# Performance work log

Hardware: AMD Instinct MI355X
Metric: run time of the kernel (lower is better)

Reference implementation:

```python
import jax, jax.numpy as jnp
import numpy as np

EPS = 1e-16  # PyG softmax denominator epsilon


def segment_softmax(alpha, batch, num_segments):
    # alpha: (n,1); softmax within each bag (PyG-style: subtract segment max)
    m = jax.ops.segment_max(alpha, batch, num_segments=num_segments)
    e = jnp.exp(alpha - m[batch])
    s = jax.ops.segment_sum(e, batch, num_segments=num_segments)
    return e / (s[batch] + EPS)


def global_softmax_pooling(x, alpha, batch, num_segments):
    a = segment_softmax(alpha, batch, num_segments)
    return jax.ops.segment_sum(x * a, batch, num_segments=num_segments)  # (B,d)


def setup_inputs() -> dict:
    key = jax.random.key(0)
    k1, k2 = jax.random.split(key)
    n, d, B = 262144, 256, 512
    x = jax.random.normal(k1, (n, d), dtype=jnp.float32)
    batch = jnp.sort(jax.random.randint(k2, (n,), 0, B))
    return {"x": x, "batch": batch, "num_segments": B}


def reference(x, batch, num_segments):
    K = 3  # module default k
    alpha = jnp.zeros((x.shape[0], 1), dtype=x.dtype)
    for _ in range(K):  # small fixed iteration count
        z = global_softmax_pooling(x, alpha, batch, num_segments)  # (B,d)
        energy = jnp.sum(z * z, axis=1, keepdims=True)  # (B,1)
        z_squashed = jnp.sqrt(energy) / (1.0 + energy) * z  # (B,d)
        # alpha_i += <x_i, z_squashed[batch_i]> (vectorizes the per-bag mm loop)
        alpha = alpha + jnp.sum(x * z_squashed[batch], axis=1, keepdims=True)
    return global_softmax_pooling(x, alpha, batch, num_segments)
```

## Files before the change

kernel.cpp:

```cpp
#include <hip/hip_runtime.h>

#define BLOCK 1024
#define D 256
#define NW 16
#define NH 32
#define ALPHA_CAP 4096

__device__ __forceinline__ unsigned bfbits(float f) {
    unsigned u = __float_as_uint(f);
    return (u + 0x7fffu + ((u >> 16) & 1u)) >> 16;
}
__device__ __forceinline__ float bflo(unsigned u) { return __uint_as_float(u << 16); }
__device__ __forceinline__ float bfhi(unsigned u) { return __uint_as_float(u & 0xffff0000u); }

template<int USE_WS>
__global__ __launch_bounds__(BLOCK, 2)
void dynpool_kernel(const float* __restrict__ x,
                    unsigned short* __restrict__ xb,
                    const int* __restrict__ batch,
                    float* __restrict__ out,
                    int n)
{
    __shared__ float alpha_s[ALPHA_CAP];
    __shared__ float zpart[NH][D];
    __shared__ float s_s[NH];
    __shared__ float zs[D];
    __shared__ float red2[NW + 2];
    __shared__ int bounds[2];

    const int tid  = threadIdx.x;
    const int s    = blockIdx.x;
    const int wv   = tid >> 6;
    const int lane = tid & 63;
    const int hw   = lane >> 5;
    const int l    = lane & 31;
    const int slot = (wv << 1) | hw;

    if (tid == 0) {
        int lo = 0, hi = n;
        while (lo < hi) { int mid = (lo + hi) >> 1; if (batch[mid] < s) lo = mid + 1; else hi = mid; }
        bounds[0] = lo;
        int lo2 = lo, hi2 = n;
        while (lo2 < hi2) { int mid = (lo2 + hi2) >> 1; if (batch[mid] < s + 1) lo2 = mid + 1; else hi2 = mid; }
        bounds[1] = lo2;
    }
    __syncthreads();
    const int start = bounds[0];
    const int cnt   = bounds[1] - bounds[0];

    if (cnt == 0) {
        if (tid < D) out[(size_t)s * D + tid] = 0.f;
        return;
    }

    for (int r = tid; r < cnt; r += BLOCK) alpha_s[r] = 0.f;

    float zr[8];
#pragma unroll
    for (int j = 0; j < 8; ++j) zr[j] = 0.f;
    __syncthreads();

    for (int iter = 0; iter < 4; ++iter) {
        float s_acc = 0.f;
        float za[8];
#pragma unroll
        for (int j = 0; j < 8; ++j) za[j] = 0.f;

        if (iter == 0) {
            for (int r = slot; r < cnt; r += NH) {
                const size_t boff = (size_t)(start + r) * D + l * 8;
                const float4 v0 = *(const float4*)(x + boff);
                const float4 v1 = *(const float4*)(x + boff + 4);
                if (USE_WS) {
                    uint4 p;
                    p.x = bfbits(v0.x) | (bfbits(v0.y) << 16);
                    p.y = bfbits(v0.z) | (bfbits(v0.w) << 16);
                    p.z = bfbits(v1.x) | (bfbits(v1.y) << 16);
                    p.w = bfbits(v1.z) | (bfbits(v1.w) << 16);
                    *(uint4*)(xb + boff) = p;
                }
                s_acc += 1.f;
                za[0] += v0.x; za[1] += v0.y; za[2] += v0.z; za[3] += v0.w;
                za[4] += v1.x; za[5] += v1.y; za[6] += v1.z; za[7] += v1.w;
            }
        } else {
            int r = slot;
            uint4 u_cur = make_uint4(0, 0, 0, 0);
            float4 f0_cur = {0,0,0,0}, f1_cur = {0,0,0,0};
            float a_cur = 0.f;
            if (r < cnt) {
                const size_t boff = (size_t)(start + r) * D + l * 8;
                if (USE_WS) u_cur = *(const uint4*)(xb + boff);
                else { f0_cur = *(const float4*)(x + boff); f1_cur = *(const float4*)(x + boff + 4); }
                a_cur = alpha_s[r];
            }
            while (r < cnt) {
                const int rn = r + NH;
                uint4 u_nxt = make_uint4(0, 0, 0, 0);
                float4 f0_nxt = {0,0,0,0}, f1_nxt = {0,0,0,0};
                float a_nxt = 0.f;
                if (rn < cnt) {
                    const size_t boffn = (size_t)(start + rn) * D + l * 8;
                    if (USE_WS) u_nxt = *(const uint4*)(xb + boffn);
                    else { f0_nxt = *(const float4*)(x + boffn); f1_nxt = *(const float4*)(x + boffn + 4); }
                    a_nxt = alpha_s[rn];
                }
                float xf[8];
                if (USE_WS) {
                    xf[0] = bflo(u_cur.x); xf[1] = bfhi(u_cur.x);
                    xf[2] = bflo(u_cur.y); xf[3] = bfhi(u_cur.y);
                    xf[4] = bflo(u_cur.z); xf[5] = bfhi(u_cur.z);
                    xf[6] = bflo(u_cur.w); xf[7] = bfhi(u_cur.w);
                } else {
                    xf[0] = f0_cur.x; xf[1] = f0_cur.y; xf[2] = f0_cur.z; xf[3] = f0_cur.w;
                    xf[4] = f1_cur.x; xf[5] = f1_cur.y; xf[6] = f1_cur.z; xf[7] = f1_cur.w;
                }
                float dt = 0.f;
#pragma unroll
                for (int j = 0; j < 8; ++j) dt += xf[j] * zr[j];
#pragma unroll
                for (int o = 16; o; o >>= 1) dt += __shfl_xor(dt, o);
                const float a_new = a_cur + dt;
                if (l == 0) alpha_s[r] = a_new;
                const float w = __expf(a_new);
                s_acc += w;
#pragma unroll
                for (int j = 0; j < 8; ++j) za[j] += w * xf[j];
                u_cur = u_nxt; f0_cur = f0_nxt; f1_cur = f1_nxt; a_cur = a_nxt;
                r = rn;
            }
        }

        if (l == 0) s_s[slot] = s_acc;
#pragma unroll
        for (int j = 0; j < 8; ++j) zpart[slot][l * 8 + j] = za[j];
        __syncthreads();

        if (tid == 0) {
            float st = 0.f;
            for (int h = 0; h < NH; ++h) st += s_s[h];
            red2[NW + 1] = 1.f / (st + 1e-16f);
        }
        __syncthreads();

        float zc = 0.f;
        if (tid < D) {
#pragma unroll
            for (int h = 0; h < NH; ++h) zc += zpart[h][tid];
            zc *= red2[NW + 1];
        }

        if (iter == 3) {
            if (tid < D) out[(size_t)s * D + tid] = zc;
            break;
        }

        float e = (tid < D) ? zc * zc : 0.f;
#pragma unroll
        for (int o = 32; o; o >>= 1) e += __shfl_xor(e, o);
        if (lane == 0) red2[wv] = e;
        __syncthreads();
        if (tid == 0) {
            float E = 0.f;
            for (int h = 0; h < NW; ++h) E += red2[h];
            red2[NW] = (E > 0.f) ? (sqrtf(E) / (1.f + E)) : 0.f;
        }
        __syncthreads();
        const float scale = red2[NW];
        if (tid < D) zs[tid] = zc * scale;
        __syncthreads();
#pragma unroll
        for (int j = 0; j < 8; ++j) zr[j] = zs[l * 8 + j];
        __syncthreads();
    }
}

extern "C" void kernel_launch(void* const* d_in, const int* in_sizes, int n_in,
                              void* d_out, int out_size, void* d_ws, size_t ws_size,
                              hipStream_t stream) {
    const float* x   = (const float*)d_in[0];
    const int* batch = (const int*)d_in[1];
    float* out       = (float*)d_out;
    const int n = in_sizes[1];
    const int B = out_size / D;
    const size_t need = (size_t)n * D * sizeof(unsigned short);
    if (ws_size >= need) {
        dynpool_kernel<1><<<B, BLOCK, 0, stream>>>(x, (unsigned short*)d_ws, batch, out, n);
    } else {
        dynpool_kernel<0><<<B, BLOCK, 0, stream>>>(x, (unsigned short*)d_ws, batch, out, n);
    }
}
```

Measured before the change: 166.9 us.

## Split fused per-bag kernel into multi-launch stream and reduce passes

Replaces the single fused kernel (one 1024-thread block per bag looping over all iterations) with alternating stream and reduce kernels. Each bag is split into 8 chunks handled by separate 256-thread blocks to raise parallelism and spread load across CUs. Per-row alpha is no longer stored; instead the cumulative squashed z vector S is accumulated, so alpha is recomputed as a single dot product against S. The cost is eight kernel launches with global round-trips for the partials, and the subtraction of the segment max is still absent.

```diff
diff --git a/kernel.cpp b/kernel.cpp
--- a/kernel.cpp
+++ b/kernel.cpp
@@ -1,10 +1,8 @@
 #include <hip/hip_runtime.h>
 
-#define BLOCK 1024
 #define D 256
-#define NW 16
-#define NH 32
-#define ALPHA_CAP 4096
+#define CPS 8
+#define TPB 256
 
 __device__ __forceinline__ unsigned bfbits(float f) {
     unsigned u = __float_as_uint(f);
@@ -13,166 +11,140 @@
 __device__ __forceinline__ float bflo(unsigned u) { return __uint_as_float(u << 16); }
 __device__ __forceinline__ float bfhi(unsigned u) { return __uint_as_float(u & 0xffff0000u); }
 
-template<int USE_WS>
-__global__ __launch_bounds__(BLOCK, 2)
-void dynpool_kernel(const float* __restrict__ x,
-                    unsigned short* __restrict__ xb,
-                    const int* __restrict__ batch,
-                    float* __restrict__ out,
-                    int n)
+template<int T0, int USE_WS>
+__global__ __launch_bounds__(TPB)
+void stream_k(const float* __restrict__ x,
+              unsigned short* __restrict__ xb,
+              const int* __restrict__ batch,
+              const float* __restrict__ S,
+              float* __restrict__ part,
+              int n)
 {
-    __shared__ float alpha_s[ALPHA_CAP];
-    __shared__ float zpart[NH][D];
-    __shared__ float s_s[NH];
-    __shared__ float zs[D];
-    __shared__ float red2[NW + 2];
+    __shared__ float zp[8][D + 4];
+    __shared__ float sp[8];
     __shared__ int bounds[2];
+    const int tid = threadIdx.x;
+    const int s   = blockIdx.x / CPS;
+    const int k   = blockIdx.x % CPS;
+    const int hw  = tid >> 5;
+    const int l   = tid & 31;
 
-    const int tid  = threadIdx.x;
-    const int s    = blockIdx.x;
-    const int wv   = tid >> 6;
-    const int lane = tid & 63;
-    const int hw   = lane >> 5;
-    const int l    = lane & 31;
-    const int slot = (wv << 1) | hw;
-
-    if (tid == 0) {
+    if (tid < 2) {
+        const int key = s + tid;
         int lo = 0, hi = n;
-        while (lo < hi) { int mid = (lo + hi) >> 1; if (batch[mid] < s) lo = mid + 1; else hi = mid; }
-        bounds[0] = lo;
-        int lo2 = lo, hi2 = n;
-        while (lo2 < hi2) { int mid = (lo2 + hi2) >> 1; if (batch[mid] < s + 1) lo2 = mid + 1; else hi2 = mid; }
-        bounds[1] = lo2;
+        while (lo < hi) { int mid = (lo + hi) >> 1; if (batch[mid] < key) lo = mid + 1; else hi = mid; }
+        bounds[tid] = lo;
     }
     __syncthreads();
     const int start = bounds[0];
     const int cnt   = bounds[1] - bounds[0];
+    const int csz   = (cnt + CPS - 1) / CPS;
+    const int rbeg  = k * csz;
+    const int rend  = min(cnt, rbeg + csz);
 
-    if (cnt == 0) {
-        if (tid < D) out[(size_t)s * D + tid] = 0.f;
-        return;
+    float zr[8];
+    if (!T0) {
+        const float4 a = *(const float4*)(S + (size_t)s * D + l * 8);
+        const float4 b = *(const float4*)(S + (size_t)s * D + l * 8 + 4);
+        zr[0]=a.x; zr[1]=a.y; zr[2]=a.z; zr[3]=a.w;
+        zr[4]=b.x; zr[5]=b.y; zr[6]=b.z; zr[7]=b.w;
+    }
+    float za[8] = {0,0,0,0,0,0,0,0};
+    float s_acc = 0.f;
+
+    for (int r = rbeg + hw; r < rend; r += 8) {
+        const size_t boff = (size_t)(start + r) * D + l * 8;
+        float xf[8];
+        if (T0) {
+            const float4 v0 = *(const float4*)(x + boff);
+            const float4 v1 = *(const float4*)(x + boff + 4);
+            xf[0]=v0.x; xf[1]=v0.y; xf[2]=v0.z; xf[3]=v0.w;
+            xf[4]=v1.x; xf[5]=v1.y; xf[6]=v1.z; xf[7]=v1.w;
+            if (USE_WS) {
+                uint4 p;
+                p.x = bfbits(xf[0]) | (bfbits(xf[1]) << 16);
+                p.y = bfbits(xf[2]) | (bfbits(xf[3]) << 16);
+                p.z = bfbits(xf[4]) | (bfbits(xf[5]) << 16);
+                p.w = bfbits(xf[6]) | (bfbits(xf[7]) << 16);
+                *(uint4*)(xb + boff) = p;
+            }
+            s_acc += 1.f;
+#pragma unroll
+            for (int j = 0; j < 8; ++j) za[j] += xf[j];
+        } else {
+            if (USE_WS) {
+                const uint4 u = *(const uint4*)(xb + boff);
+                xf[0]=bflo(u.x); xf[1]=bfhi(u.x); xf[2]=bflo(u.y); xf[3]=bfhi(u.y);
+                xf[4]=bflo(u.z); xf[5]=bfhi(u.z); xf[6]=bflo(u.w); xf[7]=bfhi(u.w);
+            } else {
+                const float4 v0 = *(const float4*)(x + boff);
+                const float4 v1 = *(const float4*)(x + boff + 4);
+                xf[0]=v0.x; xf[1]=v0.y; xf[2]=v0.z; xf[3]=v0.w;
+                xf[4]=v1.x; xf[5]=v1.y; xf[6]=v1.z; xf[7]=v1.w;
+            }
+            float dt = 0.f;
+#pragma unroll
+            for (int j = 0; j < 8; ++j) dt += xf[j] * zr[j];
+#pragma unroll
+            for (int o = 16; o; o >>= 1) dt += __shfl_xor(dt, o);
+            const float w = __expf(dt);
+            s_acc += w;
+#pragma unroll
+            for (int j = 0; j < 8; ++j) za[j] += w * xf[j];
+        }
     }
 
-    for (int r = tid; r < cnt; r += BLOCK) alpha_s[r] = 0.f;
-
-    float zr[8];
 #pragma unroll
-    for (int j = 0; j < 8; ++j) zr[j] = 0.f;
+    for (int j = 0; j < 8; ++j) zp[hw][l * 8 + j] = za[j];
+    if (l == 0) sp[hw] = s_acc;
     __syncthreads();
 
-    for (int iter = 0; iter < 4; ++iter) {
-        float s_acc = 0.f;
-        float za[8];
+    float acc = 0.f;
 #pragma unroll
-        for (int j = 0; j < 8; ++j) za[j] = 0.f;
+    for (int h = 0; h < 8; ++h) acc += zp[h][tid];
+    float* po = part + (size_t)(s * CPS + k) * (D + 1);
+    po[tid] = acc;
+    if (tid == 0) {
+        float st = 0.f;
+        for (int h = 0; h < 8; ++h) st += sp[h];
+        po[D] = st;
+    }
+}
 
-        if (iter == 0) {
-            for (int r = slot; r < cnt; r += NH) {
-                const size_t boff = (size_t)(start + r) * D + l * 8;
-                const float4 v0 = *(const float4*)(x + boff);
-                const float4 v1 = *(const float4*)(x + boff + 4);
-                if (USE_WS) {
-                    uint4 p;
-                    p.x = bfbits(v0.x) | (bfbits(v0.y) << 16);
-                    p.y = bfbits(v0.z) | (bfbits(v0.w) << 16);
-                    p.z = bfbits(v1.x) | (bfbits(v1.y) << 16);
-                    p.w = bfbits(v1.z) | (bfbits(v1.w) << 16);
-                    *(uint4*)(xb + boff) = p;
-                }
-                s_acc += 1.f;
-                za[0] += v0.x; za[1] += v0.y; za[2] += v0.z; za[3] += v0.w;
-                za[4] += v1.x; za[5] += v1.y; za[6] += v1.z; za[7] += v1.w;
-            }
-        } else {
-            int r = slot;
-            uint4 u_cur = make_uint4(0, 0, 0, 0);
-            float4 f0_cur = {0,0,0,0}, f1_cur = {0,0,0,0};
-            float a_cur = 0.f;
-            if (r < cnt) {
-                const size_t boff = (size_t)(start + r) * D + l * 8;
-                if (USE_WS) u_cur = *(const uint4*)(xb + boff);
-                else { f0_cur = *(const float4*)(x + boff); f1_cur = *(const float4*)(x + boff + 4); }
-                a_cur = alpha_s[r];
-            }
-            while (r < cnt) {
-                const int rn = r + NH;
-                uint4 u_nxt = make_uint4(0, 0, 0, 0);
-                float4 f0_nxt = {0,0,0,0}, f1_nxt = {0,0,0,0};
-                float a_nxt = 0.f;
-                if (rn < cnt) {
-                    const size_t boffn = (size_t)(start + rn) * D + l * 8;
-                    if (USE_WS) u_nxt = *(const uint4*)(xb + boffn);
-                    else { f0_nxt = *(const float4*)(x + boffn); f1_nxt = *(const float4*)(x + boffn + 4); }
-                    a_nxt = alpha_s[rn];
-                }
-                float xf[8];
-                if (USE_WS) {
-                    xf[0] = bflo(u_cur.x); xf[1] = bfhi(u_cur.x);
-                    xf[2] = bflo(u_cur.y); xf[3] = bfhi(u_cur.y);
-                    xf[4] = bflo(u_cur.z); xf[5] = bfhi(u_cur.z);
-                    xf[6] = bflo(u_cur.w); xf[7] = bfhi(u_cur.w);
-                } else {
-                    xf[0] = f0_cur.x; xf[1] = f0_cur.y; xf[2] = f0_cur.z; xf[3] = f0_cur.w;
-                    xf[4] = f1_cur.x; xf[5] = f1_cur.y; xf[6] = f1_cur.z; xf[7] = f1_cur.w;
-                }
-                float dt = 0.f;
+template<int ASSIGN, int FINAL>
+__global__ __launch_bounds__(TPB)
+void reduce_k(const float* __restrict__ part,
+              float* __restrict__ S,
+              float* __restrict__ out)
+{
+    __shared__ float red[8];
+    const int s   = blockIdx.x;
+    const int tid = threadIdx.x;
+    const float* pb = part + (size_t)s * CPS * (D + 1);
+    float zn = 0.f;
 #pragma unroll
-                for (int j = 0; j < 8; ++j) dt += xf[j] * zr[j];
+    for (int kk = 0; kk < CPS; ++kk) zn += pb[kk * (D + 1) + tid];
+    if (tid == 0) {
+        float st = 0.f;
+        for (int kk = 0; kk < CPS; ++kk) st += pb[kk * (D + 1) + D];
+        red[0] = 1.f / (st + 1e-16f);
+    }
+    __syncthreads();
+    const float z = zn * red[0];
+    if (FINAL) { out[(size_t)s * D + tid] = z; return; }
+    float e = z * z;
 #pragma unroll
-                for (int o = 16; o; o >>= 1) dt += __shfl_xor(dt, o);
-                const float a_new = a_cur + dt;
-                if (l == 0) alpha_s[r] = a_new;
-                const float w = __expf(a_new);
-                s_acc += w;
-#pragma unroll
-                for (int j = 0; j < 8; ++j) za[j] += w * xf[j];
-                u_cur = u_nxt; f0_cur = f0_nxt; f1_cur = f1_nxt; a_cur = a_nxt;
-                r = rn;
-            }
-        }
-
-        if (l == 0) s_s[slot] = s_acc;
-#pragma unroll
-        for (int j = 0; j < 8; ++j) zpart[slot][l * 8 + j] = za[j];
-        __syncthreads();
-
-        if (tid == 0) {
-            float st = 0.f;
-            for (int h = 0; h < NH; ++h) st += s_s[h];
-            red2[NW + 1] = 1.f / (st + 1e-16f);
-        }
-        __syncthreads();
-
-        float zc = 0.f;
-        if (tid < D) {
-#pragma unroll
-            for (int h = 0; h < NH; ++h) zc += zpart[h][tid];
-            zc *= red2[NW + 1];
-        }
-
-        if (iter == 3) {
-            if (tid < D) out[(size_t)s * D + tid] = zc;
-            break;
-        }
-
-        float e = (tid < D) ? zc * zc : 0.f;
-#pragma unroll
-        for (int o = 32; o; o >>= 1) e += __shfl_xor(e, o);
-        if (lane == 0) red2[wv] = e;
-        __syncthreads();
-        if (tid == 0) {
-            float E = 0.f;
-            for (int h = 0; h < NW; ++h) E += red2[h];
-            red2[NW] = (E > 0.f) ? (sqrtf(E) / (1.f + E)) : 0.f;
-        }
-        __syncthreads();
-        const float scale = red2[NW];
-        if (tid < D) zs[tid] = zc * scale;
-        __syncthreads();
-#pragma unroll
-        for (int j = 0; j < 8; ++j) zr[j] = zs[l * 8 + j];
-        __syncthreads();
+    for (int o = 32; o; o >>= 1) e += __shfl_xor(e, o);
+    if ((tid & 63) == 0) red[4 + (tid >> 6)] = e;
+    __syncthreads();
+    if (tid == 0) {
+        const float E = red[4] + red[5] + red[6] + red[7];
+        red[1] = (E > 0.f) ? (sqrtf(E) / (1.f + E)) : 0.f;
     }
+    __syncthreads();
+    const float v = z * red[1];
+    if (ASSIGN) S[(size_t)s * D + tid] = v;
+    else        S[(size_t)s * D + tid] += v;
 }
 
 extern "C" void kernel_launch(void* const* d_in, const int* in_sizes, int n_in,
@@ -183,10 +155,35 @@
     float* out       = (float*)d_out;
     const int n = in_sizes[1];
     const int B = out_size / D;
-    const size_t need = (size_t)n * D * sizeof(unsigned short);
-    if (ws_size >= need) {
-        dynpool_kernel<1><<<B, BLOCK, 0, stream>>>(x, (unsigned short*)d_ws, batch, out, n);
+
+    const size_t xb_bytes   = (size_t)n * D * sizeof(unsigned short);
+    const size_t part_elems = (size_t)B * CPS * (D + 1);
+    const size_t S_elems    = (size_t)B * D;
+    const size_t small_bytes = (part_elems + S_elems) * sizeof(float);
+    const bool use_ws = ws_size >= xb_bytes + small_bytes;
+
+    unsigned short* xb = (unsigned short*)d_ws;
+    float* part = use_ws ? (float*)((char*)d_ws + xb_bytes) : (float*)d_ws;
+    float* S    = part + part_elems;
+    const int grid = B * CPS;
+
+    if (use_ws) {
+        stream_k<1,1><<<grid, TPB, 0, stream>>>(x, xb, batch, S, part, n);
+        reduce_k<1,0><<<B, TPB, 0, stream>>>(part, S, out);
+        stream_k<0,1><<<grid, TPB, 0, stream>>>(x, xb, batch, S, part, n);
+        reduce_k<0,0><<<B, TPB, 0, stream>>>(part, S, out);
+        stream_k<0,1><<<grid, TPB, 0, stream>>>(x, xb, batch, S, part, n);
+        reduce_k<0,0><<<B, TPB, 0, stream>>>(part, S, out);
+        stream_k<0,1><<<grid, TPB, 0, stream>>>(x, xb, batch, S, part, n);
+        reduce_k<0,1><<<B, TPB, 0, stream>>>(part, S, out);
     } else {
-        dynpool_kernel<0><<<B, BLOCK, 0, stream>>>(x, (unsigned short*)d_ws, batch, out, n);
+        stream_k<1,0><<<grid, TPB, 0, stream>>>(x, xb, batch, S, part, n);
+        reduce_k<1,0><<<B, TPB, 0, stream>>>(part, S, out);
+        stream_k<0,0><<<grid, TPB, 0, stream>>>(x, xb, batch, S, part, n);
+        reduce_k<0,0><<<B, TPB, 0, stream>>>(part, S, out);
+        stream_k<0,0><<<grid, TPB, 0, stream>>>(x, xb, batch, S, part, n);
+        reduce_k<0,0><<<B, TPB, 0, stream>>>(part, S, out);
+        stream_k<0,0><<<grid, TPB, 0, stream>>>(x, xb, batch, S, part, n);
+        reduce_k<0,1><<<B, TPB, 0, stream>>>(part, S, out);
     }
 }
```

After: 188.7 us. 1.13x slower.
